# Kernel tuning notes

Hardware: AMD Instinct MI355X
Metric: run time of the kernel (lower is better)

Reference implementation:

```python
import jax, jax.numpy as jnp
import numpy as np

T = 16384
J = 21
IN = 3 * J + 278  # 341
H = 512
WIDTH = 64


def _gru_cell(x, h, w_ih, w_hh, b_ih, b_n):
    # equinox GRUCell math: igates = W_ih x + b; hgates = W_hh h
    ig = w_ih @ x + b_ih            # [3H]
    hg = w_hh @ h                   # [3H]
    ir, iz, inn = jnp.split(ig, 3)
    hr, hz, hn = jnp.split(hg, 3)
    r = jax.nn.sigmoid(ir + hr)
    z = jax.nn.sigmoid(iz + hz)
    n = jnp.tanh(inn + r * (hn + b_n))
    return n + z * (h - n)


def setup_inputs() -> dict:
    key = jax.random.key(0)
    ks = jax.random.split(key, 32)
    s = 0.02
    inp = {
        'dh_joint_pos_tj': jax.random.normal(ks[0], (T, J), jnp.float32),
        'dh_joint_vel_tj': jax.random.normal(ks[1], (T, J), jnp.float32),
        'com_inertia_tn': jax.random.normal(ks[2], (T, 160), jnp.float32),
        'com_vel_tn': jax.random.normal(ks[3], (T, 96), jnp.float32),
        'imu_acc_t3': jax.random.normal(ks[4], (T, 3), jnp.float32),
        'imu_gyro_t3': jax.random.normal(ks[5], (T, 3), jnp.float32),
        'act_frc_obs_tn': jax.random.normal(ks[6], (T, J), jnp.float32),
        'base_pos_t3': jax.random.normal(ks[7], (T, 3), jnp.float32),
        'base_quat_t4': jax.random.normal(ks[8], (T, 4), jnp.float32),
        'lin_vel_obs_t3': jax.random.normal(ks[9], (T, 3), jnp.float32),
        'ang_vel_obs_t3': jax.random.normal(ks[10], (T, 3), jnp.float32),
        'lin_vel_cmd_t2': jax.random.normal(ks[11], (T, 2), jnp.float32),
        'ang_vel_cmd_t1': jax.random.normal(ks[12], (T, 1), jnp.float32),
        'hidden_states_dn': jnp.zeros((2, H), jnp.float32),
        # GRU layer 0 (input IN -> H)
        'w_ih0': jax.random.normal(ks[13], (3 * H, IN), jnp.float32) * s,
        'w_hh0': jax.random.normal(ks[14], (3 * H, H), jnp.float32) * s,
        'b_ih0': jax.random.normal(ks[15], (3 * H,), jnp.float32) * s,
        'b_n0': jax.random.normal(ks[16], (H,), jnp.float32) * s,
        # GRU layer 1 (H -> H)
        'w_ih1': jax.random.normal(ks[17], (3 * H, H), jnp.float32) * s,
        'w_hh1': jax.random.normal(ks[18], (3 * H, H), jnp.float32) * s,
        'b_ih1': jax.random.normal(ks[19], (3 * H,), jnp.float32) * s,
        'b_n1': jax.random.normal(ks[20], (H,), jnp.float32) * s,
        # projector MLP: H -> 64 -> 64 -> 1, relu hidden activations
        'mw0': jax.random.normal(ks[21], (WIDTH, H), jnp.float32) * s,
        'mb0': jnp.zeros((WIDTH,), jnp.float32),
        'mw1': jax.random.normal(ks[22], (WIDTH, WIDTH), jnp.float32) * s,
        'mb1': jnp.zeros((WIDTH,), jnp.float32),
        'mw2': jax.random.normal(ks[23], (1, WIDTH), jnp.float32) * s,
        'mb2': jnp.zeros((1,), jnp.float32),
    }
    return inp


def reference(dh_joint_pos_tj, dh_joint_vel_tj, com_inertia_tn, com_vel_tn,
              imu_acc_t3, imu_gyro_t3, act_frc_obs_tn, base_pos_t3,
              base_quat_t4, lin_vel_obs_t3, ang_vel_obs_t3, lin_vel_cmd_t2,
              ang_vel_cmd_t1, hidden_states_dn,
              w_ih0, w_hh0, b_ih0, b_n0, w_ih1, w_hh1, b_ih1, b_n1,
              mw0, mb0, mw1, mb1, mw2, mb2):
    obs_tn = jnp.concatenate([
        dh_joint_pos_tj, dh_joint_vel_tj, com_inertia_tn, com_vel_tn,
        imu_acc_t3, imu_gyro_t3, act_frc_obs_tn, base_pos_t3, base_quat_t4,
        lin_vel_obs_t3, ang_vel_obs_t3, lin_vel_cmd_t2, ang_vel_cmd_t1,
    ], axis=-1)  # [T, 341]

    def scan_fn(carry, xt):
        h0 = _gru_cell(xt, carry[0], w_ih0, w_hh0, b_ih0, b_n0)
        h1 = _gru_cell(h0, carry[1], w_ih1, w_hh1, b_ih1, b_n1)
        v = jax.nn.relu(mw0 @ h1 + mb0)
        v = jax.nn.relu(mw1 @ v + mb1)
        yt = mw2 @ v + mb2  # [1]
        return jnp.stack([h0, h1], axis=0), yt

    new_hidden, out_tn = jax.lax.scan(scan_fn, hidden_states_dn, obs_tn)
    return out_tn, new_hidden
```

## Files before the change

### kernel.cpp

```cpp
#include <hip/hip_runtime.h>
#include <math.h>


#define T_STEPS 16384
#define IN_DIM 341
#define HID 512
#define G3 1536
#define TTILE 16
#define R0M 15
#define R1M 15
#define POLL_LIM (1<<18)

typedef unsigned int v4u __attribute__((ext_vector_type(4)));

__device__ __forceinline__ float dot4(float4 a, float4 b) {
  return fmaf(a.x, b.x, fmaf(a.y, b.y, fmaf(a.z, b.z, a.w * b.w)));
}
__device__ __forceinline__ float fast_sigmoid(float x) {
  return __builtin_amdgcn_rcpf(1.0f + __expf(-x));
}
__device__ __forceinline__ float fast_tanh(float x) {
  return fmaf(-2.0f, __builtin_amdgcn_rcpf(1.0f + __expf(2.0f * x)), 1.0f);
}
__device__ __forceinline__ void st_rlx64(unsigned long long* p, unsigned long long v) {
  __hip_atomic_store(p, v, __ATOMIC_RELAXED, __HIP_MEMORY_SCOPE_AGENT);
}
__device__ __forceinline__ unsigned long long pack_tv(unsigned tag, float v) {
  return ((unsigned long long)tag << 32) | (unsigned long long)__float_as_uint(v);
}
__device__ __forceinline__ void pin4(float4& v) {
  asm volatile("" : "+v"(v.x), "+v"(v.y), "+v"(v.z), "+v"(v.w));
}
template <int CTRL>
__device__ __forceinline__ float ror_add(float x) {
  int t = __builtin_amdgcn_update_dpp(0, __float_as_int(x), CTRL, 0xf, 0xf, true);
  return x + __int_as_float(t);
}
__device__ __forceinline__ void reduce16x3(float& pr, float& pz, float& pn) {
  pr = ror_add<0x128>(pr); pz = ror_add<0x128>(pz); pn = ror_add<0x128>(pn);
  pr = ror_add<0x124>(pr); pz = ror_add<0x124>(pz); pn = ror_add<0x124>(pn);
  pr = ror_add<0x122>(pr); pz = ror_add<0x122>(pz); pn = ror_add<0x122>(pn);
  pr = ror_add<0x121>(pr); pz = ror_add<0x121>(pz); pn = ror_add<0x121>(pn);
}
__device__ __forceinline__ v4u ld16(const unsigned long long* p) {
  v4u r;
  asm volatile("global_load_dwordx4 %0, %1, off sc0 sc1\n\ts_waitcnt vmcnt(0)"
               : "=v"(r) : "v"(p) : "memory");
  return r;
}
__device__ __forceinline__ void ld16x2(const unsigned long long* p0,
                                       const unsigned long long* p1,
                                       v4u& a, v4u& b) {
  asm volatile("global_load_dwordx4 %0, %2, off sc0 sc1\n\t"
               "global_load_dwordx4 %1, %3, off sc0 sc1\n\t"
               "s_waitcnt vmcnt(0)"
               : "=&v"(a), "=&v"(b) : "v"(p0), "v"(p1) : "memory");
}
__device__ __forceinline__ void set_abort(int* c) {
  if (c) __hip_atomic_store(c, 1, __ATOMIC_RELAXED, __HIP_MEMORY_SCOPE_AGENT);
}
__device__ __forceinline__ bool chk_abort(const int* c) {
  return c && __hip_atomic_load(c, __ATOMIC_RELAXED, __HIP_MEMORY_SCOPE_AGENT);
}
__device__ __forceinline__ bool wait_tag(const unsigned long long* p, unsigned tag,
                                         v4u& a, int* ctrl) {
  if (a.y == tag && a.w == tag) return true;
  int gd = 0;
  for (;;) {
    v4u b0, b1;
    asm volatile("global_load_dwordx4 %0, %2, off sc0 sc1\n\t"
                 "s_sleep 3\n\t"
                 "global_load_dwordx4 %1, %2, off sc0 sc1\n\t"
                 "s_waitcnt vmcnt(1)"
                 : "=&v"(b0), "=&v"(b1) : "v"(p) : "memory");
    bool ok0 = (b0.y == tag && b0.w == tag);
    asm volatile("s_waitcnt vmcnt(0)" : "+v"(b1) :: "memory");
    if (ok0) { a = b0; return true; }
    if (b1.y == tag && b1.w == tag) { a = b1; return true; }
    if (++gd >= POLL_LIM) { set_abort(ctrl); return false; }
    if ((gd & 63) == 0 && chk_abort(ctrl)) return false;
    if (gd < 16) __builtin_amdgcn_s_sleep(1);
    else         __builtin_amdgcn_s_sleep(8);
  }
}

__global__ __launch_bounds__(384) void concat_kernel(
    const float* __restrict__ p0, const float* __restrict__ p1,
    const float* __restrict__ p2, const float* __restrict__ p3,
    const float* __restrict__ p4, const float* __restrict__ p5,
    const float* __restrict__ p6, const float* __restrict__ p7,
    const float* __restrict__ p8, const float* __restrict__ p9,
    const float* __restrict__ p10, const float* __restrict__ p11,
    const float* __restrict__ p12, float* __restrict__ obs) {
  int t = blockIdx.x;
  int k = threadIdx.x;
  if (k >= IN_DIM) return;
  float v;
  if (k < 21)       v = p0[t*21 + k];
  else if (k < 42)  v = p1[t*21 + (k-21)];
  else if (k < 202) v = p2[t*160 + (k-42)];
  else if (k < 298) v = p3[t*96 + (k-202)];
  else if (k < 301) v = p4[t*3 + (k-298)];
  else if (k < 304) v = p5[t*3 + (k-301)];
  else if (k < 325) v = p6[t*21 + (k-304)];
  else if (k < 328) v = p7[t*3 + (k-325)];
  else if (k < 332) v = p8[t*4 + (k-328)];
  else if (k < 335) v = p9[t*3 + (k-332)];
  else if (k < 338) v = p10[t*3 + (k-335)];
  else if (k < 340) v = p11[t*2 + (k-338)];
  else              v = p12[t];
  obs[(size_t)t*IN_DIM + k] = v;
}

__global__ __launch_bounds__(256) void transpose_kernel(const float* __restrict__ w,
                                                        float* __restrict__ wT) {
  __shared__ float tile[32][33];
  int tx = threadIdx.x;
  int ty = threadIdx.y;
  int k = blockIdx.x*32 + tx;
#pragma unroll
  for (int jj = 0; jj < 4; jj++) {
    int r = blockIdx.y*32 + ty*4 + jj;
    tile[ty*4+jj][tx] = (k < IN_DIM) ? w[(size_t)r*IN_DIM + k] : 0.f;
  }
  __syncthreads();
#pragma unroll
  for (int jj = 0; jj < 4; jj++) {
    int kk = blockIdx.x*32 + ty*4 + jj;
    if (kk < IN_DIM) wT[(size_t)kk*G3 + blockIdx.y*32 + tx] = tile[tx][ty*4+jj];
  }
}

__global__ __launch_bounds__(256) void ig0_kernel(const float* __restrict__ wT,
                                                  const float* __restrict__ obs,
                                                  const float* __restrict__ b_ih0,
                                                  float* __restrict__ ig0) {
  int o = blockIdx.x*256 + threadIdx.x;
  int t0 = blockIdx.y * TTILE;
  float acc[TTILE];
  float b = b_ih0[o];
#pragma unroll
  for (int tt = 0; tt < TTILE; tt++) acc[tt] = b;
  for (int k = 0; k < IN_DIM; k++) {
    float wv = wT[(size_t)k*G3 + o];
#pragma unroll
    for (int tt = 0; tt < TTILE; tt++)
      acc[tt] = fmaf(obs[(size_t)(t0+tt)*IN_DIM + k], wv, acc[tt]);
  }
#pragma unroll
  for (int tt = 0; tt < TTILE; tt++)
    ig0[(size_t)(t0+tt)*G3 + o] = acc[tt];
}

__global__ __launch_bounds__(512) void init_kernel(const float* __restrict__ hid,
                                                   unsigned long long* ring0,
                                                   unsigned long long* ring1,
                                                   int* ctrl) {
  int e = threadIdx.x;
  if (e == 0 && ctrl)
    __hip_atomic_store(ctrl, 0, __ATOMIC_RELAXED, __HIP_MEMORY_SCOPE_AGENT);
  st_rlx64(&ring0[e], pack_tv(0u, hid[e]));
  st_rlx64(&ring1[e], pack_tv(0u, hid[HID + e]));
}

__global__ __launch_bounds__(384)
__attribute__((amdgpu_waves_per_eu(1, 2)))
void seq_kernel(
    const float* __restrict__ ig0, const float* __restrict__ w_hh0,
    const float* __restrict__ b_n0, const float* __restrict__ w_ih1,
    const float* __restrict__ w_hh1, const float* __restrict__ b_ih1,
    const float* __restrict__ b_n1,
    unsigned long long* ring0, unsigned long long* ring1,
    float* __restrict__ h1a, float* __restrict__ d_out, int* ctrl) {
  __shared__ float hbuf0[2][HID];
  __shared__ float hbuf1[2][HID];
  __shared__ float igbuf[2][24];
  __shared__ float vpad[24576];
  __shared__ int s_dead;
  const int tid = threadIdx.x;
  const int wg = blockIdx.x;
  if (tid == 0) s_dead = 0;
  if (d_out == nullptr) {
    vpad[tid] = (float)tid;
    __syncthreads();
    h1a[tid] = vpad[383 - tid];
  }

  const bool roleA = (tid < 128);
  const int u = tid - 128;
  const int g = roleA ? (tid >> 4) : (u >> 5);
  const int jj = roleA ? (tid & 15) : (u & 15);
  const int half = roleA ? 0 : ((u >> 4) & 1);
  const int j32 = roleA ? 0 : (u & 31);
  const int eg = wg*8 + g;
  const bool leadA = roleA && (jj == 0);
  const bool leadB = (!roleA) && (j32 == 0);

  const float* wsrc = roleA ? w_hh0 : (half ? w_hh1 : w_ih1);
  float4 W[24];
#pragma unroll
  for (int gate = 0; gate < 3; gate++) {
    const float4* row = (const float4*)(wsrc + (size_t)(gate*HID + eg)*HID);
#pragma unroll
    for (int i = 0; i < 8; i++) {
      W[gate*8+i] = row[jj + 16*i];
      pin4(W[gate*8+i]);
    }
  }
  float cr=0.f, cz=0.f, cn=0.f, bnl;
  if (roleA) {
    bnl = b_n0[eg];
  } else {
    cr = b_ih1[eg]; cz = b_ih1[512+eg]; cn = b_ih1[1024+eg]; bnl = b_n1[eg];
  }

  const int iggate = tid >> 3, ige = tid & 7;
  if (tid < 24) igbuf[0][tid] = ig0[(size_t)iggate*HID + wg*8 + ige];

  for (int k = 0; k <= T_STEPS; k++) {
    const int p = k & 1;
    float igpre = 0.f;
    if (tid < 24) {
      int kk = (k+1 < T_STEPS) ? (k+1) : (T_STEPS-1);
      igpre = ig0[(size_t)kk*G3 + (size_t)iggate*HID + wg*8 + ige];
    }
    const unsigned wk0 = (unsigned)k, wk1 = (unsigned)(k-1);
    bool ok = true;
    if (k == 0) {
      if (tid < 256) {
        const unsigned long long* pa = ring0 + 2*tid;
        v4u a = ld16(pa);
        ok = wait_tag(pa, wk0, a, ctrl);
        ((float2*)hbuf0[p])[tid] =
            make_float2(__uint_as_float(a.x), __uint_as_float(a.z));
      }
    } else {
      const unsigned long long* pa = ring0 + (size_t)(k & R0M)*HID + 2*tid;
      const unsigned long long* pb = ring1 + (size_t)((k-1) & R1M)*HID + 2*(tid-128);
      if (tid < 128) {
        v4u a = ld16(pa);
        ok = wait_tag(pa, wk0, a, ctrl);
        ((float2*)hbuf0[p])[tid] =
            make_float2(__uint_as_float(a.x), __uint_as_float(a.z));
      } else if (tid < 256) {
        v4u a, b;
        ld16x2(pa, pb, a, b);
        bool okA = wait_tag(pa, wk0, a, ctrl);
        bool okB = wait_tag(pb, wk1, b, ctrl);
        ok = okA && okB;
        ((float2*)hbuf0[p])[tid] =
            make_float2(__uint_as_float(a.x), __uint_as_float(a.z));
        ((float2*)hbuf1[p])[tid-128] =
            make_float2(__uint_as_float(b.x), __uint_as_float(b.z));
      } else {
        v4u b = ld16(pb);
        ok = wait_tag(pb, wk1, b, ctrl);
        ((float2*)hbuf1[p])[tid-128] =
            make_float2(__uint_as_float(b.x), __uint_as_float(b.z));
      }
    }
    if (!ok) s_dead = 1;
    __syncthreads();
    if (s_dead) break;
    const bool act = roleA ? (k < T_STEPS) : (k >= 1);
    if (act) {
      const float4* hp = (roleA || half == 0) ? (const float4*)hbuf0[p]
                                              : (const float4*)hbuf1[p];
      float pr=0.f, pz=0.f, pn=0.f;
#pragma unroll
      for (int i = 0; i < 8; i++) {
        float4 hv = hp[jj + 16*i];
        pr += dot4(W[i],hv); pz += dot4(W[8+i],hv); pn += dot4(W[16+i],hv);
      }
      reduce16x3(pr, pz, pn);
      if (roleA) {
        if (leadA) {
          float r = fast_sigmoid(igbuf[p][g] + pr);
          float z = fast_sigmoid(igbuf[p][8+g] + pz);
          float n = fast_tanh(igbuf[p][16+g] + r*(pn + bnl));
          float hnew = n + z*(hbuf0[p][eg] - n);
          st_rlx64(&ring0[(size_t)((k+1) & R0M)*HID + eg],
                   pack_tv((unsigned)(k+1), hnew));
          if (k == T_STEPS-1) d_out[T_STEPS + eg] = hnew;
        }
      } else {
        float qr = __shfl(pr, 16, 32);
        float qz = __shfl(pz, 16, 32);
        float qn = __shfl(pn, 16, 32);
        if (leadB) {
          float r = fast_sigmoid(pr + cr + qr);
          float z = fast_sigmoid(pz + cz + qz);
          float n = fast_tanh(pn + cn + r*(qn + bnl));
          float hnew = n + z*(hbuf1[p][eg] - n);
          st_rlx64(&ring1[(size_t)(k & R1M)*HID + eg],
                   pack_tv((unsigned)k, hnew));
          h1a[(size_t)(k-1)*HID + eg] = hnew;
          if (k == T_STEPS) d_out[T_STEPS + HID + eg] = hnew;
        }
      }
    }
    if (tid < 24) igbuf[p ^ 1][tid] = igpre;
  }
}

__global__ __launch_bounds__(64) void mlp_kernel(
    const float* __restrict__ h1_all, const float* __restrict__ mw0,
    const float* __restrict__ mb0, const float* __restrict__ mw1,
    const float* __restrict__ mb1, const float* __restrict__ mw2,
    const float* __restrict__ mb2, float* __restrict__ out) {
  const int l = threadIdx.x;
  const int t0 = blockIdx.x * 8;
  __shared__ float v0s[8][64];
  float acc[8];
#pragma unroll
  for (int tt = 0; tt < 8; tt++) acc[tt] = mb0[l];
  const float4* w = (const float4*)(mw0 + (size_t)l*512);
#pragma unroll 4
  for (int i = 0; i < 128; i++) {
    float4 a = w[i];
#pragma unroll
    for (int tt = 0; tt < 8; tt++) {
      float4 b = ((const float4*)(h1_all + (size_t)(t0+tt)*512))[i];
      acc[tt] = fmaf(a.x,b.x, fmaf(a.y,b.y, fmaf(a.z,b.z, fmaf(a.w,b.w, acc[tt]))));
    }
  }
#pragma unroll
  for (int tt = 0; tt < 8; tt++) v0s[tt][l] = fmaxf(acc[tt], 0.f);
  __syncthreads();
  float acc1[8];
#pragma unroll
  for (int tt = 0; tt < 8; tt++) acc1[tt] = mb1[l];
  const float* w1 = mw1 + (size_t)l*64;
  for (int jj = 0; jj < 64; jj++) {
    float wv = w1[jj];
#pragma unroll
    for (int tt = 0; tt < 8; tt++) acc1[tt] = fmaf(wv, v0s[tt][jj], acc1[tt]);
  }
  float w2 = mw2[l];
  float bb = mb2[0];
#pragma unroll
  for (int tt = 0; tt < 8; tt++) {
    float y = w2 * fmaxf(acc1[tt], 0.f);
#pragma unroll
    for (int s = 32; s > 0; s >>= 1) y += __shfl_down(y, s, 64);
    if (l == 0) out[t0+tt] = y + bb;
  }
}

extern "C" void kernel_launch(void* const* d_in, const int* in_sizes, int n_in,
                              void* d_out, int out_size, void* d_ws, size_t ws_size,
                              hipStream_t stream) {
  const float* p0  = (const float*)d_in[0];
  const float* p1  = (const float*)d_in[1];
  const float* p2  = (const float*)d_in[2];
  const float* p3  = (const float*)d_in[3];
  const float* p4  = (const float*)d_in[4];
  const float* p5  = (const float*)d_in[5];
  const float* p6  = (const float*)d_in[6];
  const float* p7  = (const float*)d_in[7];
  const float* p8  = (const float*)d_in[8];
  const float* p9  = (const float*)d_in[9];
  const float* p10 = (const float*)d_in[10];
  const float* p11 = (const float*)d_in[11];
  const float* p12 = (const float*)d_in[12];
  const float* hid   = (const float*)d_in[13];
  const float* w_ih0 = (const float*)d_in[14];
  const float* w_hh0 = (const float*)d_in[15];
  const float* b_ih0 = (const float*)d_in[16];
  const float* b_n0  = (const float*)d_in[17];
  const float* w_ih1 = (const float*)d_in[18];
  const float* w_hh1 = (const float*)d_in[19];
  const float* b_ih1 = (const float*)d_in[20];
  const float* b_n1  = (const float*)d_in[21];
  const float* mw0 = (const float*)d_in[22];
  const float* mb0 = (const float*)d_in[23];
  const float* mw1 = (const float*)d_in[24];
  const float* mb1 = (const float*)d_in[25];
  const float* mw2 = (const float*)d_in[26];
  const float* mb2 = (const float*)d_in[27];
  float* out = (float*)d_out;

  char* base = (char*)d_ws;
  const size_t IG0_B = (size_t)T_STEPS*G3*4;
  const size_t R0_B  = (size_t)16*HID*8;
  const size_t R1_B  = (size_t)16*HID*8;
  const size_t H1A_B = (size_t)T_STEPS*HID*4;
  const size_t TOTAL = IG0_B + R0_B + R1_B + H1A_B;
  float* ig0 = (float*)base;
  unsigned long long* ring0 = (unsigned long long*)(base + IG0_B);
  unsigned long long* ring1 = (unsigned long long*)(base + IG0_B + R0_B);
  float* h1a = (float*)(base + IG0_B + R0_B + R1_B);
  float* obs = h1a;
  float* wT  = (float*)((char*)h1a + (size_t)T_STEPS*IN_DIM*4);
  if (ws_size < TOTAL) return;
  int* ctrl = (ws_size >= TOTAL + 4096) ? (int*)(base + TOTAL) : nullptr;

  concat_kernel<<<T_STEPS, 384, 0, stream>>>(p0,p1,p2,p3,p4,p5,p6,p7,p8,p9,p10,p11,p12, obs);
  transpose_kernel<<<dim3(11,48), dim3(32,8), 0, stream>>>(w_ih0, wT);
  ig0_kernel<<<dim3(6, T_STEPS/TTILE), 256, 0, stream>>>(wT, obs, b_ih0, ig0);
  init_kernel<<<1, 512, 0, stream>>>(hid, ring0, ring1, ctrl);
  seq_kernel<<<64, 384, 0, stream>>>(ig0, w_hh0, b_n0, w_ih1, w_hh1, b_ih1, b_n1,
                                     ring0, ring1, h1a, out, ctrl);
  mlp_kernel<<<T_STEPS/8, 64, 0, stream>>>(h1a, mw0, mb0, mw1, mb1, mw2, mb2, out);
}
```

Before: 30.14 ms.

## Split GRU recurrence across 128 workgroups with 4 hidden units each

Redistributes the persistent sequential GRU kernel from 64 workgroups of 384 threads (8 hidden units each) to 128 workgroups of 256 threads (4 units each), so each workgroup does less matvec work per step. The ring-buffer gather is restructured so 128 threads each load two 16-byte entries for layer 0 and layer 1 states. The spin-wait is simplified to a single load per short sleep, and explicit vmcnt waits are added after publishing the state. The intent is a shorter per-step critical path, at the cost of more workgroups polling the ring each step, which raises cross-CU synchronisation traffic, and 64 idle threads per workgroup.

```diff
diff --git a/kernel.cpp b/kernel.cpp
--- a/kernel.cpp
+++ b/kernel.cpp
@@ -7,6 +7,8 @@
 #define HID 512
 #define G3 1536
 #define TTILE 16
+#define NWG 128
+#define EPW 4
 #define R0M 15
 #define R1M 15
 #define POLL_LIM (1<<18)
@@ -67,20 +69,11 @@
   if (a.y == tag && a.w == tag) return true;
   int gd = 0;
   for (;;) {
-    v4u b0, b1;
-    asm volatile("global_load_dwordx4 %0, %2, off sc0 sc1\n\t"
-                 "s_sleep 3\n\t"
-                 "global_load_dwordx4 %1, %2, off sc0 sc1\n\t"
-                 "s_waitcnt vmcnt(1)"
-                 : "=&v"(b0), "=&v"(b1) : "v"(p) : "memory");
-    bool ok0 = (b0.y == tag && b0.w == tag);
-    asm volatile("s_waitcnt vmcnt(0)" : "+v"(b1) :: "memory");
-    if (ok0) { a = b0; return true; }
-    if (b1.y == tag && b1.w == tag) { a = b1; return true; }
+    __builtin_amdgcn_s_sleep(1);
+    a = ld16(p);
+    if (a.y == tag && a.w == tag) return true;
     if (++gd >= POLL_LIM) { set_abort(ctrl); return false; }
-    if ((gd & 63) == 0 && chk_abort(ctrl)) return false;
-    if (gd < 16) __builtin_amdgcn_s_sleep(1);
-    else         __builtin_amdgcn_s_sleep(8);
+    if ((gd & 255) == 0 && chk_abort(ctrl)) return false;
   }
 }
 
@@ -163,7 +156,7 @@
   st_rlx64(&ring1[e], pack_tv(0u, hid[HID + e]));
 }
 
-__global__ __launch_bounds__(384)
+__global__ __launch_bounds__(256)
 __attribute__((amdgpu_waves_per_eu(1, 2)))
 void seq_kernel(
     const float* __restrict__ ig0, const float* __restrict__ w_hh0,
@@ -174,7 +167,7 @@
     float* __restrict__ h1a, float* __restrict__ d_out, int* ctrl) {
   __shared__ float hbuf0[2][HID];
   __shared__ float hbuf1[2][HID];
-  __shared__ float igbuf[2][24];
+  __shared__ float igbuf[2][12];
   __shared__ float vpad[24576];
   __shared__ int s_dead;
   const int tid = threadIdx.x;
@@ -183,86 +176,95 @@
   if (d_out == nullptr) {
     vpad[tid] = (float)tid;
     __syncthreads();
-    h1a[tid] = vpad[383 - tid];
-  }
-
-  const bool roleA = (tid < 128);
-  const int u = tid - 128;
+    h1a[tid] = vpad[255 - tid];
+  }
+
+  const bool roleA = (tid < 64);
+  const int u = tid - 64;
+  const bool roleB = (tid >= 64) && (tid < 192);
   const int g = roleA ? (tid >> 4) : (u >> 5);
   const int jj = roleA ? (tid & 15) : (u & 15);
   const int half = roleA ? 0 : ((u >> 4) & 1);
   const int j32 = roleA ? 0 : (u & 31);
-  const int eg = wg*8 + g;
+  const int eg = wg*EPW + g;
   const bool leadA = roleA && (jj == 0);
-  const bool leadB = (!roleA) && (j32 == 0);
-
-  const float* wsrc = roleA ? w_hh0 : (half ? w_hh1 : w_ih1);
+  const bool leadB = roleB && (j32 == 0);
+
   float4 W[24];
-#pragma unroll
-  for (int gate = 0; gate < 3; gate++) {
-    const float4* row = (const float4*)(wsrc + (size_t)(gate*HID + eg)*HID);
-#pragma unroll
-    for (int i = 0; i < 8; i++) {
-      W[gate*8+i] = row[jj + 16*i];
-      pin4(W[gate*8+i]);
-    }
-  }
-  float cr=0.f, cz=0.f, cn=0.f, bnl;
-  if (roleA) {
-    bnl = b_n0[eg];
-  } else {
-    cr = b_ih1[eg]; cz = b_ih1[512+eg]; cn = b_ih1[1024+eg]; bnl = b_n1[eg];
-  }
-
-  const int iggate = tid >> 3, ige = tid & 7;
-  if (tid < 24) igbuf[0][tid] = ig0[(size_t)iggate*HID + wg*8 + ige];
+  float cr=0.f, cz=0.f, cn=0.f, bnl=0.f;
+  if (tid < 192) {
+    const float* wsrc = roleA ? w_hh0 : (half ? w_hh1 : w_ih1);
+#pragma unroll
+    for (int gate = 0; gate < 3; gate++) {
+      const float4* row = (const float4*)(wsrc + (size_t)(gate*HID + eg)*HID);
+#pragma unroll
+      for (int i = 0; i < 8; i++) {
+        W[gate*8+i] = row[jj + 16*i];
+        pin4(W[gate*8+i]);
+      }
+    }
+    if (roleA) {
+      bnl = b_n0[eg];
+    } else {
+      cr = b_ih1[eg]; cz = b_ih1[512+eg]; cn = b_ih1[1024+eg]; bnl = b_n1[eg];
+    }
+  }
+
+  const int iggate = tid >> 2, ige = tid & 3;
+  if (tid < 12) igbuf[0][tid] = ig0[(size_t)iggate*HID + wg*EPW + ige];
 
   for (int k = 0; k <= T_STEPS; k++) {
     const int p = k & 1;
     float igpre = 0.f;
-    if (tid < 24) {
+    if (tid < 12) {
       int kk = (k+1 < T_STEPS) ? (k+1) : (T_STEPS-1);
-      igpre = ig0[(size_t)kk*G3 + (size_t)iggate*HID + wg*8 + ige];
+      igpre = ig0[(size_t)kk*G3 + (size_t)iggate*HID + wg*EPW + ige];
     }
     const unsigned wk0 = (unsigned)k, wk1 = (unsigned)(k-1);
     bool ok = true;
     if (k == 0) {
-      if (tid < 256) {
-        const unsigned long long* pa = ring0 + 2*tid;
-        v4u a = ld16(pa);
-        ok = wait_tag(pa, wk0, a, ctrl);
-        ((float2*)hbuf0[p])[tid] =
-            make_float2(__uint_as_float(a.x), __uint_as_float(a.z));
+      if (tid < 128) {
+        const unsigned long long* pa = ring0 + 4*tid;
+        v4u a, a2;
+        ld16x2(pa, pa+2, a, a2);
+        bool o1 = wait_tag(pa,   0u, a,  ctrl);
+        bool o2 = wait_tag(pa+2, 0u, a2, ctrl);
+        ok = o1 && o2;
+        ((float2*)hbuf0[p])[2*tid]   =
+            make_float2(__uint_as_float(a.x),  __uint_as_float(a.z));
+        ((float2*)hbuf0[p])[2*tid+1] =
+            make_float2(__uint_as_float(a2.x), __uint_as_float(a2.z));
       }
     } else {
-      const unsigned long long* pa = ring0 + (size_t)(k & R0M)*HID + 2*tid;
-      const unsigned long long* pb = ring1 + (size_t)((k-1) & R1M)*HID + 2*(tid-128);
       if (tid < 128) {
-        v4u a = ld16(pa);
-        ok = wait_tag(pa, wk0, a, ctrl);
-        ((float2*)hbuf0[p])[tid] =
-            make_float2(__uint_as_float(a.x), __uint_as_float(a.z));
-      } else if (tid < 256) {
-        v4u a, b;
-        ld16x2(pa, pb, a, b);
-        bool okA = wait_tag(pa, wk0, a, ctrl);
-        bool okB = wait_tag(pb, wk1, b, ctrl);
-        ok = okA && okB;
-        ((float2*)hbuf0[p])[tid] =
-            make_float2(__uint_as_float(a.x), __uint_as_float(a.z));
-        ((float2*)hbuf1[p])[tid-128] =
-            make_float2(__uint_as_float(b.x), __uint_as_float(b.z));
+        const unsigned long long* pa = ring0 + (size_t)(k & R0M)*HID + 4*tid;
+        v4u a, a2;
+        ld16x2(pa, pa+2, a, a2);
+        bool o1 = wait_tag(pa,   wk0, a,  ctrl);
+        bool o2 = wait_tag(pa+2, wk0, a2, ctrl);
+        ok = o1 && o2;
+        ((float2*)hbuf0[p])[2*tid]   =
+            make_float2(__uint_as_float(a.x),  __uint_as_float(a.z));
+        ((float2*)hbuf0[p])[2*tid+1] =
+            make_float2(__uint_as_float(a2.x), __uint_as_float(a2.z));
       } else {
-        v4u b = ld16(pb);
-        ok = wait_tag(pb, wk1, b, ctrl);
-        ((float2*)hbuf1[p])[tid-128] =
-            make_float2(__uint_as_float(b.x), __uint_as_float(b.z));
+        const int t1 = tid - 128;
+        const unsigned long long* pb = ring1 + (size_t)((k-1) & R1M)*HID + 4*t1;
+        v4u b, b2;
+        ld16x2(pb, pb+2, b, b2);
+        bool o1 = wait_tag(pb,   wk1, b,  ctrl);
+        bool o2 = wait_tag(pb+2, wk1, b2, ctrl);
+        ok = o1 && o2;
+        ((float2*)hbuf1[p])[2*t1]   =
+            make_float2(__uint_as_float(b.x),  __uint_as_float(b.z));
+        ((float2*)hbuf1[p])[2*t1+1] =
+            make_float2(__uint_as_float(b2.x), __uint_as_float(b2.z));
       }
     }
     if (!ok) s_dead = 1;
     __syncthreads();
     if (s_dead) break;
-    const bool act = roleA ? (k < T_STEPS) : (k >= 1);
+    const bool act = roleA ? (k < T_STEPS) : (roleB && k >= 1);
     if (act) {
       const float4* hp = (roleA || half == 0) ? (const float4*)hbuf0[p]
                                               : (const float4*)hbuf1[p];
@@ -276,11 +278,12 @@
       if (roleA) {
         if (leadA) {
           float r = fast_sigmoid(igbuf[p][g] + pr);
-          float z = fast_sigmoid(igbuf[p][8+g] + pz);
-          float n = fast_tanh(igbuf[p][16+g] + r*(pn + bnl));
+          float z = fast_sigmoid(igbuf[p][4+g] + pz);
+          float n = fast_tanh(igbuf[p][8+g] + r*(pn + bnl));
           float hnew = n + z*(hbuf0[p][eg] - n);
           st_rlx64(&ring0[(size_t)((k+1) & R0M)*HID + eg],
                    pack_tv((unsigned)(k+1), hnew));
+          asm volatile("s_waitcnt vmcnt(0)" ::: "memory");
           if (k == T_STEPS-1) d_out[T_STEPS + eg] = hnew;
         }
       } else {
@@ -294,12 +297,13 @@
           float hnew = n + z*(hbuf1[p][eg] - n);
           st_rlx64(&ring1[(size_t)(k & R1M)*HID + eg],
                    pack_tv((unsigned)k, hnew));
+          asm volatile("s_waitcnt vmcnt(0)" ::: "memory");
           h1a[(size_t)(k-1)*HID + eg] = hnew;
           if (k == T_STEPS) d_out[T_STEPS + HID + eg] = hnew;
         }
       }
     }
-    if (tid < 24) igbuf[p ^ 1][tid] = igpre;
+    if (tid < 12) igbuf[p ^ 1][tid] = igpre;
   }
 }
 
@@ -399,7 +403,7 @@
   transpose_kernel<<<dim3(11,48), dim3(32,8), 0, stream>>>(w_ih0, wT);
   ig0_kernel<<<dim3(6, T_STEPS/TTILE), 256, 0, stream>>>(wT, obs, b_ih0, ig0);
   init_kernel<<<1, 512, 0, stream>>>(hid, ring0, ring1, ctrl);
-  seq_kernel<<<64, 384, 0, stream>>>(ig0, w_hh0, b_n0, w_ih1, w_hh1, b_ih1, b_n1,
-                                     ring0, ring1, h1a, out, ctrl);
+  seq_kernel<<<NWG, 256, 0, stream>>>(ig0, w_hh0, b_n0, w_ih1, w_hh1, b_ih1, b_n1,
+                                      ring0, ring1, h1a, out, ctrl);
   mlp_kernel<<<T_STEPS/8, 64, 0, stream>>>(h1a, mw0, mb0, mw1, mb1, mw2, mb2, out);
 }
```

After: 46.52 ms. 54.4% more time.
